# Performance work log

Measured on AMD Instinct MI355X. Metric: run time of the kernel, lower is better.

The kernel has to match this reference:

```python
import jax, jax.numpy as jnp
import numpy as np
from jax import lax

L, H, R, V = 2, 1024, 3, 32000
B, T = 16, 256
EPS = 1e-6


def _layer_norm(x, gamma, beta):
    mean = jnp.mean(x, axis=-1, keepdims=True)
    sigma = jnp.sqrt(jnp.mean(jnp.square(x - mean), axis=-1, keepdims=True))
    return gamma * ((x - mean) / (sigma + EPS)) + beta


def setup_inputs() -> dict:
    key = jax.random.key(0)
    ks = jax.random.split(key, 8)
    s = 0.02  # init scale for stable activations
    inp = {
        "E": jax.random.normal(ks[0], (V, H), jnp.float32) * s,
        "ln_gamma": jnp.ones((L, H), jnp.float32),
        "ln_beta": jnp.zeros((L, H), jnp.float32),
        "Wm_k": jax.random.normal(ks[1], (L, R, H, H), jnp.float32) * s,
        "Wm_b": jnp.zeros((L, R, H), jnp.float32),
        "Wh_k": jax.random.normal(ks[2], (L, 2 * H, H), jnp.float32) * s,
        "Wh_b": jnp.zeros((L, H), jnp.float32),
        "bh": jnp.zeros((L, H), jnp.float32),
        "Wy_k": jax.random.normal(ks[3], (L, H, H), jnp.float32) * s,
        "Wy_b": jnp.zeros((L, H), jnp.float32),
        "by": jnp.zeros((L, H), jnp.float32),
        "W1_k": jax.random.normal(ks[4], (L, H, 4 * H), jnp.float32) * s,
        "W1_b": jnp.zeros((L, 4 * H), jnp.float32),
        "W2_k": jax.random.normal(ks[5], (L, 4 * H, H), jnp.float32) * s,
        "W2_b": jnp.zeros((L, H), jnp.float32),
        "x": jax.random.randint(ks[6], (B, T), 0, V, dtype=jnp.int32),
    }
    return inp


def _decode(E, ln_gamma, ln_beta, Wm_k, Wm_b, Wh_k, Wh_b, bh,
            Wy_k, Wy_b, by, W1_k, W1_b, W2_k, W2_b, x):
    x_emb = E[x]                            # [B, T, H]
    xs = jnp.transpose(x_emb, (1, 0, 2))    # [T, B, H] time-major
    h0 = jnp.zeros((L, x.shape[0], H), x_emb.dtype)

    def cell(x_curr, h_prev, m):
        x_norm = _layer_norm(x_curr, ln_gamma[m], ln_beta[m])
        x_mog, h_mog = x_norm, h_prev
        for rd in range(R):  # mogrifier rounds
            if rd % 2 == 0:
                h_mog = h_mog * (2.0 * jax.nn.sigmoid(x_mog @ Wm_k[m, rd] + Wm_b[m, rd]))
            else:
                x_mog = x_mog * (2.0 * jax.nn.sigmoid(h_mog @ Wm_k[m, rd] + Wm_b[m, rd]))
        x_conc = jnp.concatenate([x_mog, h_mog], axis=1)  # [B, 2H]
        h_curr = jnp.tanh(x_conc @ Wh_k[m] + Wh_b[m] + bh[m])
        y_curr = h_curr @ Wy_k[m] + Wy_b[m] + by[m]
        y_ffwd = jax.nn.relu(x_norm @ W1_k[m] + W1_b[m]) @ W2_k[m] + W2_b[m]
        return h_curr, x_curr + y_curr + y_ffwd  # dropout inactive (inference)

    def step(h, x_t):
        h_new = []
        prev_input = 0.0
        layer_input = x_t
        for m in range(L):
            hm, out = cell(layer_input, h[m], m)
            h_new.append(hm)
            out = out + prev_input  # res_conn across layers
            prev_input = layer_input
            layer_input = out
        return jnp.stack(h_new, axis=0), layer_input

    _, outs = lax.scan(step, h0, xs)            # outs: [T, B, H]
    dec_states = jnp.transpose(outs, (1, 0, 2))  # [B, T, H]
    return jnp.einsum('bth,vh->btv', dec_states, E)  # tied-embedding logits


def reference(E, ln_gamma, ln_beta, Wm_k, Wm_b, Wh_k, Wh_b, bh,
              Wy_k, Wy_b, by, W1_k, W1_b, W2_k, W2_b, x):
    return _decode(E, ln_gamma, ln_beta, Wm_k, Wm_b, Wh_k, Wh_b, bh,
                   Wy_k, Wy_b, by, W1_k, W1_b, W2_k, W2_b, x)
```

## Files before the change

### kernel.cpp

```cpp
#include <hip/hip_runtime.h>
#include <cstdint>
#include <cstring>
#include <cstddef>

#define L_ 2
#define H_ 1024
#define V_ 32000
#define B_ 16
#define T_ 256
#define BT_ 4096
#define EPS_ 1e-6f
#define NMID 96
#define GRID_ (16 + NMID + 16)

typedef __attribute__((ext_vector_type(8))) short bf16x8;
typedef __attribute__((ext_vector_type(4))) short s16x4;
typedef __attribute__((ext_vector_type(4))) float f32x4;
typedef __attribute__((ext_vector_type(4))) int   i32x4;

__device__ __forceinline__ short f2bf(float f){
  uint32_t u; __builtin_memcpy(&u,&f,4);
  u += 0x7fffu + ((u>>16)&1u);
  return (short)(u>>16);
}
__device__ __forceinline__ float bf2f(short s){
  uint32_t u = ((uint32_t)(unsigned short)s)<<16;
  float f; __builtin_memcpy(&f,&u,4); return f;
}
__device__ __forceinline__ unsigned pack2(short a, short b){
  return (unsigned)(unsigned short)a | ((unsigned)(unsigned short)b << 16);
}

__device__ __forceinline__ void ld_sc_x4v(const void* p, i32x4* d){
  asm volatile(
    "global_load_dwordx4 %0, %4, off sc0 sc1\n\t"
    "global_load_dwordx4 %1, %4, off offset:16 sc0 sc1\n\t"
    "global_load_dwordx4 %2, %4, off offset:32 sc0 sc1\n\t"
    "global_load_dwordx4 %3, %4, off offset:48 sc0 sc1\n\t"
    "s_waitcnt vmcnt(0)"
    : "=&v"(d[0]),"=&v"(d[1]),"=&v"(d[2]),"=&v"(d[3])
    : "v"(p) : "memory");
}
__device__ __forceinline__ unsigned ld_sc_u32(const void* p){
  unsigned r;
  asm volatile("global_load_dword %0, %1, off sc0 sc1\n\ts_waitcnt vmcnt(0)"
               : "=&v"(r) : "v"(p) : "memory");
  return r;
}
__device__ __forceinline__ void st_sc_u32(void* p, unsigned v){
  asm volatile("global_store_dword %0, %1, off sc0 sc1" :: "v"(p), "v"(v) : "memory");
}
__device__ __forceinline__ void st_sc_x4(void* p, i32x4 v){
  asm volatile("global_store_dwordx4 %0, %1, off sc0 sc1" :: "v"(p), "v"(v) : "memory");
}
__device__ __forceinline__ void drain_vm(){
  asm volatile("s_waitcnt vmcnt(0)" ::: "memory");
}

__device__ __forceinline__ void wait_flags16(const unsigned* f){
  if(threadIdx.x < 64){
    const unsigned* p = f + (threadIdx.x & 15);
    while(ld_sc_u32(p)==0u) __builtin_amdgcn_s_sleep(1);
  }
  __syncthreads();
}
__device__ __forceinline__ void wait_flag1(const unsigned* f){
  if(threadIdx.x < 64){
    while(ld_sc_u32(f)==0u) __builtin_amdgcn_s_sleep(1);
  }
  __syncthreads();
}

__device__ __forceinline__ float block_sum256(float v, float* s4){
#pragma unroll
  for(int o=32;o;o>>=1) v += __shfl_down(v,o,64);
  int lane = threadIdx.x & 63, w = threadIdx.x >> 6;
  if(lane==0) s4[w]=v;
  __syncthreads();
  float r = s4[0]+s4[1]+s4[2]+s4[3];
  __syncthreads();
  return r;
}

__global__ __launch_bounds__(256) void k_embed_ln(
    const float* __restrict__ E, const int* __restrict__ tok,
    const float* __restrict__ g, const float* __restrict__ b,
    short* __restrict__ x_emb_bf, short* __restrict__ xn_bf){
  __shared__ float s4[4];
  int row = blockIdx.x;
  int t = row >> 4, bb = row & 15;
  int tk = tok[bb*T_ + t];
  float4 v = ((const float4*)(E + (size_t)tk*H_))[threadIdx.x];
  float mean = block_sum256(v.x+v.y+v.z+v.w, s4) * (1.0f/H_);
  float d0=v.x-mean,d1=v.y-mean,d2=v.z-mean,d3=v.w-mean;
  float var = block_sum256(d0*d0+d1*d1+d2*d2+d3*d3, s4) * (1.0f/H_);
  float inv = 1.0f/(sqrtf(var)+EPS_);
  int c = threadIdx.x*4;
  s16x4 eb = {f2bf(v.x),f2bf(v.y),f2bf(v.z),f2bf(v.w)};
  ((s16x4*)(x_emb_bf + (size_t)row*H_))[threadIdx.x] = eb;
  s16x4 ob = {f2bf(g[c+0]*(d0*inv)+b[c+0]), f2bf(g[c+1]*(d1*inv)+b[c+1]),
              f2bf(g[c+2]*(d2*inv)+b[c+2]), f2bf(g[c+3]*(d3*inv)+b[c+3])};
  ((s16x4*)(xn_bf + (size_t)row*H_))[threadIdx.x] = ob;
}

__global__ __launch_bounds__(256) void k_transpose_bf(
    const float* __restrict__ src, short* __restrict__ dst, int Rr, int Cc){
  __shared__ float tile[32][33];
  int c0 = blockIdx.x*32, r0 = blockIdx.y*32;
  int tx = threadIdx.x & 31, ty = threadIdx.x >> 5;
#pragma unroll
  for(int i=0;i<32;i+=8)
    tile[ty+i][tx] = src[(size_t)(r0+ty+i)*Cc + c0+tx];
  __syncthreads();
#pragma unroll
  for(int i=0;i<32;i+=8)
    dst[(size_t)(c0+ty+i)*Rr + r0+tx] = f2bf(tile[tx][ty+i]);
}

__global__ void k_f2bf_vec(const float* __restrict__ s, short* __restrict__ d, int n4){
  int i = blockIdx.x*blockDim.x + threadIdx.x;
  int st = gridDim.x*blockDim.x;
  for(; i<n4; i+=st){
    float4 v = ((const float4*)s)[i];
    s16x4 o = {f2bf(v.x),f2bf(v.y),f2bf(v.z),f2bf(v.w)};
    ((s16x4*)d)[i] = o;
  }
}

template<int ACT, int OBF, int REMAP>
__global__ __launch_bounds__(256) void k_mfma_nt(
    const short* __restrict__ A, const short* __restrict__ Wt,
    const float* __restrict__ b1, const float* __restrict__ b2,
    const float* __restrict__ rf, const short* __restrict__ rb1,
    const short* __restrict__ rb2, void* __restrict__ out,
    int M, int N, int K){
  int wid = threadIdx.x >> 6, lane = threadIdx.x & 63;
  int m0 = blockIdx.y*64;
  int n0 = blockIdx.x*128 + wid*32;
  int lr = lane & 15, kq = lane >> 4;
  const short* Ap = A + (size_t)(m0+lr)*K + kq*8;
  const short* Bp = Wt + (size_t)(n0+lr)*K + kq*8;
  f32x4 acc[4][2];
#pragma unroll
  for(int i=0;i<4;i++)
#pragma unroll
    for(int j=0;j<2;j++) acc[i][j] = (f32x4)0.0f;
  for(int k=0;k<K;k+=32){
    bf16x8 a[4], b[2];
#pragma unroll
    for(int mi=0;mi<4;mi++) a[mi] = *(const bf16x8*)(Ap + (size_t)mi*16*K + k);
#pragma unroll
    for(int ni=0;ni<2;ni++) b[ni] = *(const bf16x8*)(Bp + (size_t)ni*16*K + k);
#pragma unroll
    for(int mi=0;mi<4;mi++)
#pragma unroll
      for(int ni=0;ni<2;ni++)
        acc[mi][ni] = __builtin_amdgcn_mfma_f32_16x16x32_bf16(a[mi], b[ni], acc[mi][ni], 0,0,0);
  }
#pragma unroll
  for(int mi=0;mi<4;mi++)
#pragma unroll
    for(int ni=0;ni<2;ni++)
#pragma unroll
      for(int r=0;r<4;r++){
        int row = m0 + mi*16 + kq*4 + r;
        int col = n0 + ni*16 + lr;
        float s = acc[mi][ni][r];
        if(b1) s += b1[col];
        if(b2) s += b2[col];
        if(ACT==1) s = 2.0f/(1.0f+expf(-s));
        else if(ACT==2) s = fmaxf(s, 0.0f);
        if(rf)  s += rf[(size_t)row*N+col];
        if(rb1) s += bf2f(rb1[(size_t)row*N+col]);
        if(rb2) s += bf2f(rb2[(size_t)row*N+col]);
        size_t orow = REMAP ? ((size_t)(row&15)*T_ + (row>>4)) : (size_t)row;
        if(OBF) ((short*)out)[orow*N+col] = f2bf(s);
        else    ((float*)out)[orow*N+col] = s;
      }
}

struct MegaArgs {
  const short *xn0, *mg0;
  const short *WmT;
  const float *Wmb;
  const short *WhT;
  const float *Whb, *bh;
  const short *WyT;
  const float *Wyb, *by;
  const short *xemb, *ff0;
  const float *lng, *lnb;
  float *out0;
  short *xn1, *g1;
  short *h0, *h1;
  short *xcat0, *xcat1;
  short *h0_all, *h1_all;
  unsigned *fA0,*fB0,*fC0,*fA1,*fB1,*fC1,*dM;
};

struct RArgs {
  const short *xn, *gate, *Wm1T, *Wm2T, *WhT;
  const float *bm1, *bm2, *bh1, *bh2;
  short *h, *xcat, *h_all;
  unsigned *fA, *fB, *fC; const unsigned* dM;
};

#define RED(buf, ksv, c, re) buf[((((ksv)*4)+((c)>>4))*16 + (re))*16 + ((c)&15)]
#define SWI(row,e) ((e) ^ (((row)&7)<<3))

template<int SC>
__device__ void recur_group(const RArgs& A, int blk, char* smem){
  short* x2   = (short*)smem;
  float* red1 = (float*)(smem + 32768);
  float* red3 = (float*)(smem + 40960);
  const int tid=threadIdx.x, w=tid>>6, lane=tid&63, lr=lane&15, kq=lane>>4;
  const int cg=w&3, ks=w>>2;
  const int wcol = blk*64 + cg*16;
  const int re = tid>>5, cp = tid&31, c0 = cp*2, c1 = c0+1, gc0 = blk*64 + c0;
  const int rl = tid>>5, seg = tid&31;
  float p3_0=0.f, p3_1=0.f;

  for(int t=0;t<T_;++t){
    const short* xn_t = A.xn + (size_t)t*16384;
    const short* g_t  = A.gate + (size_t)t*16384;
    if(SC) wait_flag1(A.dM + t);
    if(t)  wait_flags16(A.fC + (size_t)(t-1)*16);
    {
      i32x4 hv[4], gv[4];
      ld_sc_x4v(A.h + (size_t)rl*1024 + seg*32, hv);
      if(SC) ld_sc_x4v(g_t + (size_t)rl*1024 + seg*32, gv);
      else { const i32x4* gp = (const i32x4*)(g_t + (size_t)rl*1024 + seg*32);
             gv[0]=gp[0]; gv[1]=gp[1]; gv[2]=gp[2]; gv[3]=gp[3]; }
#pragma unroll
      for(int u=0;u<4;u++){
        bf16x8 h8,g8,pr;
        __builtin_memcpy(&h8,&hv[u],16); __builtin_memcpy(&g8,&gv[u],16);
#pragma unroll
        for(int j=0;j<8;j++) pr[j] = f2bf(bf2f(h8[j])*bf2f(g8[j]));
        int e = seg*32+u*8;
        *(bf16x8*)(x2 + (size_t)rl*1024 + SWI(rl,e)) = pr;
      }
    }
    __syncthreads();
    {
      f32x4 acc = (f32x4)0.0f;
#pragma unroll
      for(int kk=0;kk<16;kk++){
        int k = ks*512 + kk*32 + kq*8;
        bf16x8 a = *(const bf16x8*)(x2 + (size_t)lr*1024 + SWI(lr,k));
        bf16x8 b = *(const bf16x8*)(A.Wm1T + (size_t)(wcol+lr)*1024 + k);
        acc = __builtin_amdgcn_mfma_f32_16x16x32_bf16(a,b,acc,0,0,0);
      }
#pragma unroll
      for(int r=0;r<4;r++) RED(red1,ks,cg*16+lr,kq*4+r) = acc[r];
    }
    __syncthreads();
    {
      float z0 = RED(red1,0,c0,re) + RED(red1,1,c0,re);
      float z1 = RED(red1,0,c1,re) + RED(red1,1,c1,re);
      float ga0 = 2.f/(1.f+expf(-(z0 + A.bm1[gc0])));
      float ga1 = 2.f/(1.f+expf(-(z1 + A.bm1[gc0+1])));
      unsigned xp;
      if(SC) xp = ld_sc_u32(xn_t + (size_t)re*1024 + gc0);
      else   xp = *(const unsigned*)(xn_t + (size_t)re*1024 + gc0);
      float x0 = bf2f((short)(xp&0xffff)), x1 = bf2f((short)(xp>>16));
      st_sc_u32(A.xcat + (size_t)re*2048 + gc0, pack2(f2bf(x0*ga0), f2bf(x1*ga1)));
    }
    drain_vm(); __syncthreads();
    if(tid==0) st_sc_u32(A.fA + (size_t)t*16 + blk, 1u);
    wait_flags16(A.fA + (size_t)t*16);
    unsigned hp = ld_sc_u32(A.h + (size_t)re*1024 + gc0);
    unsigned gp2;
    if(SC) gp2 = ld_sc_u32(g_t + (size_t)re*1024 + gc0);
    else   gp2 = *(const unsigned*)(g_t + (size_t)re*1024 + gc0);
    {
      i32x4 xv[4]; ld_sc_x4v(A.xcat + (size_t)rl*2048 + seg*32, xv);
#pragma unroll
      for(int u=0;u<4;u++)
        *(i32x4*)(x2 + (size_t)rl*1024 + SWI(rl,seg*32+u*8)) = xv[u];
    }
    __syncthreads();
    {
      f32x4 acc2=(f32x4)0.0f, acc3=(f32x4)0.0f;
#pragma unroll
      for(int kk=0;kk<16;kk++){
        int k = ks*512 + kk*32 + kq*8;
        bf16x8 a  = *(const bf16x8*)(x2 + (size_t)lr*1024 + SWI(lr,k));
        bf16x8 b2 = *(const bf16x8*)(A.Wm2T + (size_t)(wcol+lr)*1024 + k);
        bf16x8 b3 = *(const bf16x8*)(A.WhT  + (size_t)(wcol+lr)*2048 + k);
        acc2 = __builtin_amdgcn_mfma_f32_16x16x32_bf16(a,b2,acc2,0,0,0);
        acc3 = __builtin_amdgcn_mfma_f32_16x16x32_bf16(a,b3,acc3,0,0,0);
      }
#pragma unroll
      for(int r=0;r<4;r++){
        RED(red1,ks,cg*16+lr,kq*4+r) = acc2[r];
        RED(red3,ks,cg*16+lr,kq*4+r) = acc3[r];
      }
    }
    __syncthreads();
    {
      float z0 = RED(red1,0,c0,re) + RED(red1,1,c0,re);
      float z1 = RED(red1,0,c1,re) + RED(red1,1,c1,re);
      p3_0 = RED(red3,0,c0,re) + RED(red3,1,c0,re);
      p3_1 = RED(red3,0,c1,re) + RED(red3,1,c1,re);
      float ga0 = 2.f/(1.f+expf(-(z0 + A.bm2[gc0])));
      float ga1 = 2.f/(1.f+expf(-(z1 + A.bm2[gc0+1])));
      float hv0 = bf2f((short)(hp&0xffff)) * bf2f((short)(gp2&0xffff)) * ga0;
      float hv1 = bf2f((short)(hp>>16))    * bf2f((short)(gp2>>16))    * ga1;
      st_sc_u32(A.xcat + (size_t)re*2048 + 1024 + gc0, pack2(f2bf(hv0), f2bf(hv1)));
    }
    drain_vm(); __syncthreads();
    if(tid==0) st_sc_u32(A.fB + (size_t)t*16 + blk, 1u);
    wait_flags16(A.fB + (size_t)t*16);
    {
      i32x4 xv[4]; ld_sc_x4v(A.xcat + (size_t)rl*2048 + 1024 + seg*32, xv);
#pragma unroll
      for(int u=0;u<4;u++)
        *(i32x4*)(x2 + (size_t)rl*1024 + SWI(rl,seg*32+u*8)) = xv[u];
    }
    __syncthreads();
    {
      f32x4 acc = (f32x4)0.0f;
#pragma unroll
      for(int kk=0;kk<16;kk++){
        int k = ks*512 + kk*32 + kq*8;
        bf16x8 a = *(const bf16x8*)(x2 + (size_t)lr*1024 + SWI(lr,k));
        bf16x8 b = *(const bf16x8*)(A.WhT + (size_t)(wcol+lr)*2048 + 1024 + k);
        acc = __builtin_amdgcn_mfma_f32_16x16x32_bf16(a,b,acc,0,0,0);
      }
#pragma unroll
      for(int r=0;r<4;r++) RED(red1,ks,cg*16+lr,kq*4+r) = acc[r];
    }
    __syncthreads();
    {
      float z0 = RED(red1,0,c0,re) + RED(red1,1,c0,re) + p3_0 + A.bh1[gc0]   + A.bh2[gc0];
      float z1 = RED(red1,0,c1,re) + RED(red1,1,c1,re) + p3_1 + A.bh1[gc0+1] + A.bh2[gc0+1];
      unsigned pk = pack2(f2bf(tanhf(z0)), f2bf(tanhf(z1)));
      st_sc_u32(A.h + (size_t)re*1024 + gc0, pk);
      st_sc_u32(A.h_all + (size_t)t*16384 + (size_t)re*1024 + gc0, pk);
    }
    drain_vm(); __syncthreads();
    if(tid==0) st_sc_u32(A.fC + (size_t)t*16 + blk, 1u);
  }
}

__device__ void middle_group(const MegaArgs& M, int m, char* smem){
  short* stash   = (short*)smem;
  short* staging = (short*)(smem + 32768);
  const size_t H2 = (size_t)H_*H_;
  const short* WgT = M.WmT + 3*H2;
  const float* bm0 = M.Wmb + 3*H_;
  const int tid=threadIdx.x, w=tid>>6, lane=tid&63, lr=lane&15, kq=lane>>4;
  const int rl=tid>>5, seg=tid&31;
  const int wc = w*128;
  for(int t=m; t<T_; t+=NMID){
    wait_flags16(M.fC0 + (size_t)t*16);
    {
      i32x4 hv[4]; ld_sc_x4v(M.h0_all + (size_t)t*16384 + (size_t)rl*1024 + seg*32, hv);
#pragma unroll
      for(int u=0;u<4;u++)
        *(i32x4*)(stash + (size_t)rl*1024 + SWI(rl,seg*32+u*8)) = hv[u];
    }
    __syncthreads();
    {
      f32x4 acc[8];
#pragma unroll
      for(int n=0;n<8;n++) acc[n]=(f32x4)0.0f;
      for(int kk=0;kk<32;kk++){
        int k = kk*32 + kq*8;
        bf16x8 a = *(const bf16x8*)(stash + (size_t)lr*1024 + SWI(lr,k));
#pragma unroll
        for(int n=0;n<8;n++){
          bf16x8 b = __builtin_nontemporal_load(
              (const bf16x8*)(M.WyT + (size_t)(wc+n*16+lr)*1024 + k));
          acc[n] = __builtin_amdgcn_mfma_f32_16x16x32_bf16(a,b,acc[n],0,0,0);
        }
      }
#pragma unroll
      for(int n=0;n<8;n++)
#pragma unroll
        for(int r=0;r<4;r++){
          int row = kq*4+r, col = wc+n*16+lr;
          size_t gi = (size_t)t*16384 + (size_t)row*1024 + col;
          float v = acc[n][r] + M.Wyb[col] + M.by[col]
                  + bf2f(__builtin_nontemporal_load(M.xemb + gi))
                  + bf2f(__builtin_nontemporal_load(M.ff0 + gi));
          __builtin_nontemporal_store(v, M.out0 + gi);
        }
    }
    drain_vm(); __syncthreads();
#pragma unroll
    for(int rr=0; rr<2; rr++){
      int row = w*2+rr;
      const float* orow = M.out0 + (size_t)t*16384 + (size_t)row*1024;
      float pv[16];
#pragma unroll
      for(int i2=0;i2<4;i2++){
        float4 v4 = *(const float4*)(orow + lane*16 + i2*4);
        pv[i2*4+0]=v4.x; pv[i2*4+1]=v4.y; pv[i2*4+2]=v4.z; pv[i2*4+3]=v4.w;
      }
      float s=0.f,q=0.f;
#pragma unroll
      for(int i=0;i<16;i++){ s += pv[i]; q += pv[i]*pv[i]; }
#pragma unroll
      for(int o=32;o;o>>=1){ s += __shfl_down(s,o,64); q += __shfl_down(q,o,64); }
      s = __shfl(s,0,64); q = __shfl(q,0,64);
      float mu = s*(1.f/1024.f);
      float sg = sqrtf(fmaxf(q*(1.f/1024.f) - mu*mu, 0.f));
      float inv = 1.f/(sg + EPS_);
      short xb[16];
#pragma unroll
      for(int i=0;i<16;i++){
        int c = lane*16+i;
        xb[i] = f2bf(M.lng[c]*((pv[i]-mu)*inv) + M.lnb[c]);
      }
      i32x4 v0, v1;
#pragma unroll
      for(int j=0;j<4;j++){
        v0[j] = (int)pack2(xb[2*j],   xb[2*j+1]);
        v1[j] = (int)pack2(xb[8+2*j], xb[9+2*j]);
      }
      short* xrow = M.xn1 + (size_t)t*16384 + (size_t)row*1024;
      st_sc_x4(xrow + lane*16, v0);
      st_sc_x4(xrow + lane*16 + 8, v1);
      *(i32x4*)(stash + (size_t)row*1024 + SWI(row,lane*16))   = v0;
      *(i32x4*)(stash + (size_t)row*1024 + SWI(row,lane*16+8)) = v1;
    }
    __syncthreads();
    {
      f32x4 acg[8];
#pragma unroll
      for(int n=0;n<8;n++) acg[n]=(f32x4)0.0f;
      for(int kk=0;kk<32;kk++){
        int k = kk*32 + kq*8;
        bf16x8 a = *(const bf16x8*)(stash + (size_t)lr*1024 + SWI(lr,k));
#pragma unroll
        for(int n=0;n<8;n++){
          bf16x8 b = __builtin_nontemporal_load(
              (const bf16x8*)(WgT + (size_t)(wc+n*16+lr)*1024 + k));
          acg[n] = __builtin_amdgcn_mfma_f32_16x16x32_bf16(a,b,acg[n],0,0,0);
        }
      }
#pragma unroll
      for(int n=0;n<8;n++)
#pragma unroll
        for(int r=0;r<4;r++){
          int row = kq*4+r, col = wc+n*16+lr;
          float gte = 2.f/(1.f+expf(-(acg[n][r] + bm0[col])));
          staging[(size_t)row*1024 + col] = f2bf(gte);
        }
    }
    __syncthreads();
    {
      short* grow = M.g1 + (size_t)t*16384 + (size_t)rl*1024 + seg*32;
#pragma unroll
      for(int u=0;u<4;u++){
        i32x4 g4 = *(const i32x4*)(staging + (size_t)rl*1024 + seg*32 + u*8);
        st_sc_x4(grow + u*8, g4);
      }
    }
    drain_vm(); __syncthreads();
    if(tid==0) st_sc_u32(M.dM + t, 1u);
  }
}

__global__ __launch_bounds__(512,1) void k_mega(MegaArgs M){
  __shared__ char smem[65536];
  const size_t H2 = (size_t)H_*H_;
  int b = blockIdx.x;
  if(b < 16){
    RArgs R{M.xn0, M.mg0, M.WmT+1*H2, M.WmT+2*H2, M.WhT,
            M.Wmb+1*H_, M.Wmb+2*H_, M.Whb, M.bh,
            M.h0, M.xcat0, M.h0_all, M.fA0, M.fB0, M.fC0, nullptr};
    recur_group<0>(R, b, smem);
  } else if(b < 16+NMID){
    middle_group(M, b-16, smem);
  } else {
    RArgs R{M.xn1, M.g1, M.WmT+4*H2, M.WmT+5*H2, M.WhT+2*H2,
            M.Wmb+4*H_, M.Wmb+5*H_, M.Whb+H_, M.bh+H_,
            M.h1, M.xcat1, M.h1_all, M.fA1, M.fB1, M.fC1, M.dM};
    recur_group<1>(R, b-(16+NMID), smem);
  }
}

extern "C" void kernel_launch(void* const* d_in, const int* in_sizes, int n_in,
                              void* d_out, int out_size, void* d_ws, size_t ws_size,
                              hipStream_t stream){
  const float* E    = (const float*)d_in[0];
  const float* ln_g = (const float*)d_in[1];
  const float* ln_b = (const float*)d_in[2];
  const float* Wm   = (const float*)d_in[3];
  const float* Wmb  = (const float*)d_in[4];
  const float* Wh   = (const float*)d_in[5];
  const float* Whb  = (const float*)d_in[6];
  const float* bh   = (const float*)d_in[7];
  const float* Wy   = (const float*)d_in[8];
  const float* Wyb  = (const float*)d_in[9];
  const float* by   = (const float*)d_in[10];
  const float* W1   = (const float*)d_in[11];
  const float* W1b  = (const float*)d_in[12];
  const float* W2   = (const float*)d_in[13];
  const float* W2b  = (const float*)d_in[14];
  const int*   xx   = (const int*)d_in[15];
  float* outF = (float*)d_out;
  (void)in_sizes; (void)n_in; (void)out_size; (void)ws_size;

  const size_t H2 = (size_t)H_*H_;
  char* p = (char*)d_ws;
  auto alloc = [&](size_t bytes)->void*{ void* r=(void*)p; p += (bytes+255)&~(size_t)255; return r; };

  short* x_emb_bf = (short*)alloc((size_t)BT_*H_*2);
  short* xn0_bf   = (short*)alloc((size_t)BT_*H_*2);
  short* mg0_bf   = (short*)alloc((size_t)BT_*H_*2);
  short* ff0_bf   = (short*)alloc((size_t)BT_*H_*2);
  float* out0     = (float*)alloc((size_t)BT_*H_*4);
  short* xn1_bf   = (short*)alloc((size_t)BT_*H_*2);
  short* g1_bf    = (short*)alloc((size_t)BT_*H_*2);
  short* ffy1r_bf = (short*)alloc((size_t)BT_*H_*2);
  short* h0_all   = (short*)alloc((size_t)BT_*H_*2);
  short* h1_all   = (short*)alloc((size_t)BT_*H_*2);
  short* dec_bf   = (short*)alloc((size_t)BT_*H_*2);
  char*  z0    = p;
  short* h0    = (short*)alloc((size_t)16*H_*2);
  short* h1    = (short*)alloc((size_t)16*H_*2);
  short* xcat0 = (short*)alloc((size_t)16*2*H_*2);
  short* xcat1 = (short*)alloc((size_t)16*2*H_*2);
  unsigned* fA0 = (unsigned*)alloc((size_t)T_*16*4);
  unsigned* fB0 = (unsigned*)alloc((size_t)T_*16*4);
  unsigned* fC0 = (unsigned*)alloc((size_t)T_*16*4);
  unsigned* fA1 = (unsigned*)alloc((size_t)T_*16*4);
  unsigned* fB1 = (unsigned*)alloc((size_t)T_*16*4);
  unsigned* fC1 = (unsigned*)alloc((size_t)T_*16*4);
  unsigned* dM  = (unsigned*)alloc((size_t)T_*4);
  size_t zbytes = (size_t)(p - z0);
  char*  wreg = p;
  short* WmT = (short*)alloc(6*H2*2);
  short* WhT = (short*)alloc(2*(size_t)H_*2*H_*2);
  short* WyT = (short*)alloc(2*H2*2);
  short* W1T = (short*)alloc(2*(size_t)4*H_*H_*2);
  short* W2T = (short*)alloc(2*(size_t)H_*4*H_*2);
  short* t1  = (short*)alloc((size_t)1024*4*H_*2);
  short* E_bf = (short*)wreg;

  hipMemsetAsync(z0, 0, zbytes, stream);

  k_embed_ln<<<BT_,256,0,stream>>>(E, xx, ln_g, ln_b, x_emb_bf, xn0_bf);
  for(int i=0;i<6;i++)
    k_transpose_bf<<<dim3(32,32),256,0,stream>>>(Wm+i*H2, WmT+i*H2, H_, H_);
  for(int l=0;l<2;l++){
    k_transpose_bf<<<dim3(32,64),256,0,stream>>>(Wh+(size_t)l*2*H2, WhT+(size_t)l*2*H2, 2*H_, H_);
    k_transpose_bf<<<dim3(32,32),256,0,stream>>>(Wy+(size_t)l*H2, WyT+(size_t)l*H2, H_, H_);
    k_transpose_bf<<<dim3(128,32),256,0,stream>>>(W1+(size_t)l*4*H2, W1T+(size_t)l*4*H2, H_, 4*H_);
    k_transpose_bf<<<dim3(32,128),256,0,stream>>>(W2+(size_t)l*4*H2, W2T+(size_t)l*4*H2, 4*H_, H_);
  }
  k_mfma_nt<1,1,0><<<dim3(8,64),256,0,stream>>>(xn0_bf, WmT, Wmb, nullptr,
      nullptr,nullptr,nullptr, mg0_bf, BT_, H_, H_);
  for(int cb=0;cb<4;cb++){
    k_mfma_nt<2,1,0><<<dim3(32,16),256,0,stream>>>(xn0_bf+(size_t)cb*1024*H_, W1T, W1b, nullptr,
        nullptr,nullptr,nullptr, t1, 1024, 4*H_, H_);
    k_mfma_nt<0,1,0><<<dim3(8,16),256,0,stream>>>(t1, W2T, W2b, nullptr,
        nullptr,nullptr,nullptr, ff0_bf+(size_t)cb*1024*H_, 1024, H_, 4*H_);
  }

  MegaArgs MA{};
  MA.xn0=xn0_bf; MA.mg0=mg0_bf;
  MA.WmT=WmT; MA.Wmb=Wmb; MA.WhT=WhT; MA.Whb=Whb; MA.bh=bh;
  MA.WyT=WyT; MA.Wyb=Wyb; MA.by=by;
  MA.xemb=x_emb_bf; MA.ff0=ff0_bf;
  MA.lng=ln_g+H_; MA.lnb=ln_b+H_;
  MA.out0=out0; MA.xn1=xn1_bf; MA.g1=g1_bf;
  MA.h0=h0; MA.h1=h1; MA.xcat0=xcat0; MA.xcat1=xcat1;
  MA.h0_all=h0_all; MA.h1_all=h1_all;
  MA.fA0=fA0; MA.fB0=fB0; MA.fC0=fC0; MA.fA1=fA1; MA.fB1=fB1; MA.fC1=fC1; MA.dM=dM;
  k_mega<<<GRID_,512,0,stream>>>(MA);

  for(int cb=0;cb<4;cb++){
    k_mfma_nt<2,1,0><<<dim3(32,16),256,0,stream>>>(xn1_bf+(size_t)cb*1024*H_, W1T+(size_t)4*H2, W1b+4*H_, nullptr,
        nullptr,nullptr,nullptr, t1, 1024, 4*H_, H_);
    k_mfma_nt<0,1,0><<<dim3(8,16),256,0,stream>>>(t1, W2T+(size_t)4*H2, W2b+H_, nullptr,
        out0+(size_t)cb*1024*H_, x_emb_bf+(size_t)cb*1024*H_, nullptr,
        ffy1r_bf+(size_t)cb*1024*H_, 1024, H_, 4*H_);
  }

  k_mfma_nt<0,1,0><<<dim3(8,64),256,0,stream>>>(h1_all, WyT+H2, Wyb+H_, by+H_,
      nullptr, ffy1r_bf, nullptr, dec_bf, BT_, H_, H_);

  k_f2bf_vec<<<2048,256,0,stream>>>(E, E_bf, (V_*H_)/4);
  k_mfma_nt<0,0,1><<<dim3(V_/128, BT_/64),256,0,stream>>>(dec_bf, E_bf, nullptr, nullptr,
      nullptr,nullptr,nullptr, outF, BT_, V_, H_);
}
```

Measured before the change: 9.376 ms.

## Fuse layer-1 FFN and output projection into mega kernel middle blocks

The separate post-recurrence launches for the layer-1 FFN (W1/ReLU/W2 with residuals) and the Wy projection are removed. That work now runs per timestep inside the idle middle-group blocks of the persistent kernel, overlapping with the recurrence. The blocks wait on the layer-1 hidden-state flags before the Wy step, and each block gets a per-block scratch buffer for the FFN intermediate. In exchange, each timestep's 16-row GEMMs re-stream the full W1/W2/Wy weights. Waiting on layer-1 flags could also delay these blocks' next gate computation.

```diff
diff --git a/kernel.cpp b/kernel.cpp
--- a/kernel.cpp
+++ b/kernel.cpp
@@ -189,6 +189,12 @@
   const float *Wyb, *by;
   const short *xemb, *ff0;
   const float *lng, *lnb;
+  const short *W1T1;
+  const float *W1b1;
+  const short *W2T1;
+  const float *W2b1;
+  short *t4s;
+  short *dec;
   float *out0;
   short *xn1, *g1;
   short *h0, *h1;
@@ -349,9 +355,13 @@
   const size_t H2 = (size_t)H_*H_;
   const short* WgT = M.WmT + 3*H2;
   const float* bm0 = M.Wmb + 3*H_;
+  const short* WyT1 = M.WyT + H2;
+  const float* Wyb1 = M.Wyb + H_;
+  const float* by1  = M.by + H_;
   const int tid=threadIdx.x, w=tid>>6, lane=tid&63, lr=lane&15, kq=lane>>4;
   const int rl=tid>>5, seg=tid&31;
   const int wc = w*128;
+  short* t4p = M.t4s + (size_t)m*(16*4096);
   for(int t=m; t<T_; t+=NMID){
     wait_flags16(M.fC0 + (size_t)t*16);
     {
@@ -460,6 +470,93 @@
     }
     drain_vm(); __syncthreads();
     if(tid==0) st_sc_u32(M.dM + t, 1u);
+    for(int nc=0;nc<4;nc++){
+      f32x4 acc[8];
+#pragma unroll
+      for(int n=0;n<8;n++) acc[n]=(f32x4)0.0f;
+      for(int kk=0;kk<32;kk++){
+        int k = kk*32 + kq*8;
+        bf16x8 a = *(const bf16x8*)(stash + (size_t)lr*1024 + SWI(lr,k));
+#pragma unroll
+        for(int n=0;n<8;n++){
+          int col = w*512 + nc*128 + n*16 + lr;
+          bf16x8 b = __builtin_nontemporal_load(
+              (const bf16x8*)(M.W1T1 + (size_t)col*1024 + k));
+          acc[n] = __builtin_amdgcn_mfma_f32_16x16x32_bf16(a,b,acc[n],0,0,0);
+        }
+      }
+#pragma unroll
+      for(int n=0;n<8;n++)
+#pragma unroll
+        for(int r=0;r<4;r++){
+          int row = kq*4+r, col = w*512 + nc*128 + n*16 + lr;
+          float v = fmaxf(acc[n][r] + M.W1b1[col], 0.f);
+          __builtin_nontemporal_store(f2bf(v), t4p + (size_t)row*4096 + col);
+        }
+    }
+    drain_vm(); __syncthreads();
+    {
+      f32x4 acc[8];
+#pragma unroll
+      for(int n=0;n<8;n++) acc[n]=(f32x4)0.0f;
+      for(int kk=0;kk<128;kk++){
+        int k = kk*32 + kq*8;
+        bf16x8 a = __builtin_nontemporal_load(
+            (const bf16x8*)(t4p + (size_t)lr*4096 + k));
+#pragma unroll
+        for(int n=0;n<8;n++){
+          bf16x8 b = __builtin_nontemporal_load(
+              (const bf16x8*)(M.W2T1 + (size_t)(wc+n*16+lr)*4096 + k));
+          acc[n] = __builtin_amdgcn_mfma_f32_16x16x32_bf16(a,b,acc[n],0,0,0);
+        }
+      }
+#pragma unroll
+      for(int n=0;n<8;n++)
+#pragma unroll
+        for(int r=0;r<4;r++){
+          int row = kq*4+r, col = wc+n*16+lr;
+          size_t gi = (size_t)t*16384 + (size_t)row*1024 + col;
+          float v = acc[n][r] + M.W2b1[col]
+                  + __builtin_nontemporal_load(M.out0 + gi)
+                  + bf2f(__builtin_nontemporal_load(M.xemb + gi));
+          staging[(size_t)row*1024 + col] = f2bf(v);
+        }
+    }
+    __syncthreads();
+    wait_flags16(M.fC1 + (size_t)t*16);
+    {
+      i32x4 hv[4]; ld_sc_x4v(M.h1_all + (size_t)t*16384 + (size_t)rl*1024 + seg*32, hv);
+#pragma unroll
+      for(int u=0;u<4;u++)
+        *(i32x4*)(stash + (size_t)rl*1024 + SWI(rl,seg*32+u*8)) = hv[u];
+    }
+    __syncthreads();
+    {
+      f32x4 acc[8];
+#pragma unroll
+      for(int n=0;n<8;n++) acc[n]=(f32x4)0.0f;
+      for(int kk=0;kk<32;kk++){
+        int k = kk*32 + kq*8;
+        bf16x8 a = *(const bf16x8*)(stash + (size_t)lr*1024 + SWI(lr,k));
+#pragma unroll
+        for(int n=0;n<8;n++){
+          bf16x8 b = __builtin_nontemporal_load(
+              (const bf16x8*)(WyT1 + (size_t)(wc+n*16+lr)*1024 + k));
+          acc[n] = __builtin_amdgcn_mfma_f32_16x16x32_bf16(a,b,acc[n],0,0,0);
+        }
+      }
+#pragma unroll
+      for(int n=0;n<8;n++)
+#pragma unroll
+        for(int r=0;r<4;r++){
+          int row = kq*4+r, col = wc+n*16+lr;
+          size_t gi = (size_t)t*16384 + (size_t)row*1024 + col;
+          float v = acc[n][r] + Wyb1[col] + by1[col]
+                  + bf2f(staging[(size_t)row*1024 + col]);
+          __builtin_nontemporal_store(f2bf(v), M.dec + gi);
+        }
+    }
+    drain_vm(); __syncthreads();
   }
 }
 
@@ -515,10 +612,10 @@
   float* out0     = (float*)alloc((size_t)BT_*H_*4);
   short* xn1_bf   = (short*)alloc((size_t)BT_*H_*2);
   short* g1_bf    = (short*)alloc((size_t)BT_*H_*2);
-  short* ffy1r_bf = (short*)alloc((size_t)BT_*H_*2);
   short* h0_all   = (short*)alloc((size_t)BT_*H_*2);
   short* h1_all   = (short*)alloc((size_t)BT_*H_*2);
   short* dec_bf   = (short*)alloc((size_t)BT_*H_*2);
+  short* t4s      = (short*)alloc((size_t)NMID*16*4096*2);
   char*  z0    = p;
   short* h0    = (short*)alloc((size_t)16*H_*2);
   short* h1    = (short*)alloc((size_t)16*H_*2);
@@ -567,23 +664,15 @@
   MA.WyT=WyT; MA.Wyb=Wyb; MA.by=by;
   MA.xemb=x_emb_bf; MA.ff0=ff0_bf;
   MA.lng=ln_g+H_; MA.lnb=ln_b+H_;
+  MA.W1T1=W1T+(size_t)4*H2; MA.W1b1=W1b+4*H_;
+  MA.W2T1=W2T+(size_t)4*H2; MA.W2b1=W2b+H_;
+  MA.t4s=t4s; MA.dec=dec_bf;
   MA.out0=out0; MA.xn1=xn1_bf; MA.g1=g1_bf;
   MA.h0=h0; MA.h1=h1; MA.xcat0=xcat0; MA.xcat1=xcat1;
   MA.h0_all=h0_all; MA.h1_all=h1_all;
   MA.fA0=fA0; MA.fB0=fB0; MA.fC0=fC0; MA.fA1=fA1; MA.fB1=fB1; MA.fC1=fC1; MA.dM=dM;
   k_mega<<<GRID_,512,0,stream>>>(MA);
 
-  for(int cb=0;cb<4;cb++){
-    k_mfma_nt<2,1,0><<<dim3(32,16),256,0,stream>>>(xn1_bf+(size_t)cb*1024*H_, W1T+(size_t)4*H2, W1b+4*H_, nullptr,
-        nullptr,nullptr,nullptr, t1, 1024, 4*H_, H_);
-    k_mfma_nt<0,1,0><<<dim3(8,16),256,0,stream>>>(t1, W2T+(size_t)4*H2, W2b+H_, nullptr,
-        out0+(size_t)cb*1024*H_, x_emb_bf+(size_t)cb*1024*H_, nullptr,
-        ffy1r_bf+(size_t)cb*1024*H_, 1024, H_, 4*H_);
-  }
-
-  k_mfma_nt<0,1,0><<<dim3(8,64),256,0,stream>>>(h1_all, WyT+H2, Wyb+H_, by+H_,
-      nullptr, ffy1r_bf, nullptr, dec_bf, BT_, H_, H_);
-
   k_f2bf_vec<<<2048,256,0,stream>>>(E, E_bf, (V_*H_)/4);
   k_mfma_nt<0,0,1><<<dim3(V_/128, BT_/64),256,0,stream>>>(dec_bf, E_bf, nullptr, nullptr,
       nullptr,nullptr,nullptr, outF, BT_, V_, H_);
```

New measurement: 10.21 ms. 8.9% more time.
